# Optimization experiments

Measured on AMD Instinct MI355X. Metric: run time of the kernel, lower is better.

The kernel has to match this reference:

```python
import jax, jax.numpy as jnp
import numpy as np

SEQ = 4096
BLOCK = 64            # sparse_block_size
BLOCKS = SEQ // BLOCK # 64 block rows/cols
NUM_ORACLES = 32
ORACLE = SEQ // NUM_ORACLES      # 128
LOCAL_BLOCKS = ORACLE // BLOCK   # 2 (sliding-window width in blocks)
PATTERN_ID = 0


def _build_block_mask(pattern_id=PATTERN_ID):
    # Mirrors DKernelPredefinedSparseAttention.__init__ create_mask((i,))
    q_pos = np.arange(BLOCKS)[:, None]
    k_pos = np.arange(BLOCKS)[None, :]
    causal = q_pos >= k_pos
    sliding = (q_pos - k_pos) < LOCAL_BLOCKS
    vert = np.zeros(BLOCKS, dtype=bool)
    real_col = int(pattern_id * ORACLE + 0.5)
    cs = real_col // BLOCK
    ce = (real_col + ORACLE) // BLOCK
    vert[cs:ce] = True
    vert[0:1] = True  # global block 0 always visible
    return causal & (sliding | vert[None, :])


def setup_inputs() -> dict:
    key = jax.random.key(0)
    kq, kk, kv = jax.random.split(key, 3)
    shape = (1, SEQ, 8, 128)  # bshd, matches module's own smoke test layout
    q = jax.random.normal(kq, shape, dtype=jnp.float32)
    k = jax.random.normal(kk, shape, dtype=jnp.float32)
    v = jax.random.normal(kv, shape, dtype=jnp.float32)
    block_mask = jnp.asarray(_build_block_mask())  # [BLOCKS, BLOCKS] bool
    return {"q": q, "k": k, "v": v, "block_mask": block_mask}


def reference(q, k, v, block_mask):
    # Expand block-level mask to token level: [S, S]
    tok_mask = jnp.repeat(jnp.repeat(block_mask, BLOCK, axis=0), BLOCK, axis=1)
    scale = 1.0 / jnp.sqrt(jnp.asarray(q.shape[-1], q.dtype))
    # bshd x bshd -> bhqk scores
    scores = jnp.einsum("bqhd,bkhd->bhqk", q, k) * scale
    neg = jnp.asarray(-1e30, scores.dtype)
    scores = jnp.where(tok_mask[None, None, :, :], scores, neg)
    probs = jax.nn.softmax(scores, axis=-1)
    out = jnp.einsum("bhqk,bkhd->bqhd", probs, v)
    return out
```

## Files before the change

### kernel.cpp

```cpp
#include <hip/hip_runtime.h>
#include <hip/hip_bf16.h>

typedef __bf16 bf16x8 __attribute__((ext_vector_type(8)));
typedef float floatx4 __attribute__((ext_vector_type(4)));

constexpr int SEQ = 4096;
constexpr int NH  = 8;
constexpr int DH  = 128;
constexpr int BLK = 64;
constexpr int QBLOCKS = SEQ / BLK;
constexpr int RS = NH * DH;
constexpr float SCALE = 0.088388347648318447f;

__device__ __forceinline__ bf16x8 load8f(const float* p) {
    float4 a = *(const float4*)p;
    float4 b = *(const float4*)(p + 4);
    bf16x8 r = { (__bf16)a.x, (__bf16)a.y, (__bf16)a.z, (__bf16)a.w,
                 (__bf16)b.x, (__bf16)b.y, (__bf16)b.z, (__bf16)b.w };
    return r;
}

__device__ __forceinline__ void stage_v(const float* __restrict__ V,
                                        int kb, int h, int n_t, int kh,
                                        __bf16* __restrict__ dst) {
    const float* base = V + (size_t)(kb * BLK + kh * 32) * RS + h * DH + n_t;
    const int nt = n_t >> 4;
    const int lbase = n_t & 15;
#pragma unroll
    for (int g = 0; g < 4; ++g) {
        bf16x8 pk;
#pragma unroll
        for (int j = 0; j < 8; ++j)
            pk[j] = (__bf16)base[(size_t)(g * 8 + j) * RS];
        __bf16* d = dst + ((size_t)((kh * 8 + nt) * 64 + lbase + 16 * g)) * 8;
        *(bf16x8*)d = pk;
    }
}

__global__ __launch_bounds__(256) void sparse_attn_kernel(
    const float* __restrict__ Q,
    const float* __restrict__ K,
    const float* __restrict__ V,
    float* __restrict__ Out)
{
    const int qb   = blockIdx.x;
    const int h    = blockIdx.y;
    const int tid  = threadIdx.x;
    const int wave = tid >> 6;
    const int lane = tid & 63;
    const int quad = lane >> 4;
    const int l16  = lane & 15;

    __shared__ __align__(16) __bf16 v_lds[2][2][8][64][8];
    __shared__ __align__(16) __bf16 p_lds[4][16][BLK + 8];

    const int n_t = tid & 127;
    const int kh  = tid >> 7;

    const int qrow = qb * BLK + wave * 16 + l16;
    const float* qp = Q + (size_t)qrow * RS + h * DH;
    bf16x8 qfrag[4];
#pragma unroll
    for (int s = 0; s < 4; ++s)
        qfrag[s] = load8f(qp + s * 32 + quad * 8);

    floatx4 o_acc[8];
#pragma unroll
    for (int n = 0; n < 8; ++n) o_acc[n] = floatx4{0.f, 0.f, 0.f, 0.f};
    float m_run[4], l_run[4];
#pragma unroll
    for (int r = 0; r < 4; ++r) { m_run[r] = -1e30f; l_run[r] = 0.f; }

    int blist[4];
    int nb = 0;
    {
        int cand[4] = {0, 1, qb - 1, qb};
        for (int i = 0; i < 4; ++i) {
            int b = cand[i];
            if (b < 0 || b > qb) continue;
            bool dup = false;
            for (int j = 0; j < nb; ++j) dup = dup || (blist[j] == b);
            if (!dup) blist[nb++] = b;
        }
    }

    stage_v(V, blist[0], h, n_t, kh, &v_lds[0][0][0][0][0]);

    for (int bi = 0; bi < nb; ++bi) {
        __syncthreads();
        if (bi + 1 < nb)
            stage_v(V, blist[bi + 1], h, n_t, kh,
                    &v_lds[(bi + 1) & 1][0][0][0][0]);

        const int kb  = blist[bi];
        const int buf = bi & 1;

        floatx4 sfrag[4];
#pragma unroll
        for (int n = 0; n < 4; ++n) {
            floatx4 c = floatx4{0.f, 0.f, 0.f, 0.f};
            const float* kp =
                K + (size_t)(kb * BLK + n * 16 + l16) * RS + h * DH;
#pragma unroll
            for (int s = 0; s < 4; ++s) {
                bf16x8 kf = load8f(kp + s * 32 + quad * 8);
                c = __builtin_amdgcn_mfma_f32_16x16x32_bf16(qfrag[s], kf, c, 0, 0, 0);
            }
            sfrag[n] = c;
        }

        float mnew[4];
#pragma unroll
        for (int r = 0; r < 4; ++r) {
            float mx = m_run[r];
#pragma unroll
            for (int n = 0; n < 4; ++n) {
                sfrag[n][r] *= SCALE;
                mx = fmaxf(mx, sfrag[n][r]);
            }
#pragma unroll
            for (int off = 1; off < 16; off <<= 1)
                mx = fmaxf(mx, __shfl_xor(mx, off, 64));
            mnew[r] = mx;
        }
#pragma unroll
        for (int r = 0; r < 4; ++r) {
            float alpha = __expf(m_run[r] - mnew[r]);
            float rs = 0.f;
#pragma unroll
            for (int n = 0; n < 4; ++n) {
                float p = __expf(sfrag[n][r] - mnew[r]);
                sfrag[n][r] = p;
                rs += p;
            }
#pragma unroll
            for (int off = 1; off < 16; off <<= 1)
                rs += __shfl_xor(rs, off, 64);
            l_run[r] = l_run[r] * alpha + rs;
            m_run[r] = mnew[r];
#pragma unroll
            for (int n = 0; n < 8; ++n) o_acc[n][r] *= alpha;
        }

#pragma unroll
        for (int n = 0; n < 4; ++n)
#pragma unroll
            for (int r = 0; r < 4; ++r)
                p_lds[wave][quad * 4 + r][n * 16 + l16] = (__bf16)sfrag[n][r];

#pragma unroll
        for (int s2 = 0; s2 < 2; ++s2) {
            bf16x8 pa = *(const bf16x8*)&p_lds[wave][l16][s2 * 32 + quad * 8];
#pragma unroll
            for (int n = 0; n < 8; ++n) {
                bf16x8 vb = *(const bf16x8*)&v_lds[buf][s2][n][lane][0];
                o_acc[n] = __builtin_amdgcn_mfma_f32_16x16x32_bf16(pa, vb, o_acc[n], 0, 0, 0);
            }
        }
    }

    const int orow_base = qb * BLK + wave * 16 + quad * 4;
#pragma unroll
    for (int r = 0; r < 4; ++r) {
        float inv = 1.f / l_run[r];
        float* op = Out + (size_t)(orow_base + r) * RS + h * DH + l16;
#pragma unroll
        for (int n = 0; n < 8; ++n)
            op[n * 16] = o_acc[n][r] * inv;
    }
}

extern "C" void kernel_launch(void* const* d_in, const int* in_sizes, int n_in,
                              void* d_out, int out_size, void* d_ws, size_t ws_size,
                              hipStream_t stream) {
    const float* Q = (const float*)d_in[0];
    const float* K = (const float*)d_in[1];
    const float* V = (const float*)d_in[2];
    float* Out = (float*)d_out;

    dim3 grid(QBLOCKS, NH);
    dim3 block(256);
    sparse_attn_kernel<<<grid, block, 0, stream>>>(Q, K, V, Out);
}
```

Before: 125.9 us.

## Split KV blocks across two wave groups per workgroup and merge partial softmax

Doubles the workgroup to 512 threads and splits the up-to-four visible key blocks between two groups of four waves. Each group keeps its own online-softmax state, and the partial outputs are merged through LDS at the end. This shortens the serial per-workgroup loop over key blocks, which matters because the grid has only 512 workgroups. In exchange it drops the double-buffered V prefetch, adds a combine step with extra LDS traffic and barriers, and each Q row is loaded by both groups.

```diff
diff --git a/kernel.cpp b/kernel.cpp
--- a/kernel.cpp
+++ b/kernel.cpp
@@ -12,6 +12,8 @@
 constexpr int RS = NH * DH;
 constexpr float SCALE = 0.088388347648318447f;
 
+constexpr int SMEM_BYTES = 51200;
+
 __device__ __forceinline__ bf16x8 load8f(const float* p) {
     float4 a = *(const float4*)p;
     float4 b = *(const float4*)(p + 4);
@@ -37,7 +39,7 @@
     }
 }
 
-__global__ __launch_bounds__(256) void sparse_attn_kernel(
+__global__ __launch_bounds__(512, 4) void sparse_attn_kernel(
     const float* __restrict__ Q,
     const float* __restrict__ K,
     const float* __restrict__ V,
@@ -47,17 +49,24 @@
     const int h    = blockIdx.y;
     const int tid  = threadIdx.x;
     const int wave = tid >> 6;
+    const int g    = wave >> 2;
+    const int ws   = wave & 3;
     const int lane = tid & 63;
     const int quad = lane >> 4;
     const int l16  = lane & 15;
 
-    __shared__ __align__(16) __bf16 v_lds[2][2][8][64][8];
-    __shared__ __align__(16) __bf16 p_lds[4][16][BLK + 8];
-
-    const int n_t = tid & 127;
-    const int kh  = tid >> 7;
-
-    const int qrow = qb * BLK + wave * 16 + l16;
+    __shared__ __align__(16) char smem[SMEM_BYTES];
+    __bf16* v_g    = (__bf16*)(smem + g * 16384);
+    __bf16* p_w    = (__bf16*)(smem + 32768 + wave * 2304);
+    float*  comb_O = (float*)smem;
+    float*  comb_m = (float*)(smem + 33792);
+    float*  comb_l = (float*)(smem + 34048);
+
+    const int tg  = tid & 255;
+    const int n_t = tg & 127;
+    const int kh  = tg >> 7;
+
+    const int qrow = qb * BLK + ws * 16 + l16;
     const float* qp = Q + (size_t)qrow * RS + h * DH;
     bf16x8 qfrag[4];
 #pragma unroll
@@ -84,89 +93,110 @@
         }
     }
 
-    stage_v(V, blist[0], h, n_t, kh, &v_lds[0][0][0][0][0]);
-
-    for (int bi = 0; bi < nb; ++bi) {
+#pragma unroll 1
+    for (int t = 0; t < 2; ++t) {
+        const int s    = 2 * g + t;
+        const bool valid = (s < nb);
+        const int kb   = valid ? blist[s] : 0;
+
+        if (valid) stage_v(V, kb, h, n_t, kh, v_g);
         __syncthreads();
-        if (bi + 1 < nb)
-            stage_v(V, blist[bi + 1], h, n_t, kh,
-                    &v_lds[(bi + 1) & 1][0][0][0][0]);
-
-        const int kb  = blist[bi];
-        const int buf = bi & 1;
-
-        floatx4 sfrag[4];
-#pragma unroll
-        for (int n = 0; n < 4; ++n) {
-            floatx4 c = floatx4{0.f, 0.f, 0.f, 0.f};
-            const float* kp =
-                K + (size_t)(kb * BLK + n * 16 + l16) * RS + h * DH;
-#pragma unroll
-            for (int s = 0; s < 4; ++s) {
-                bf16x8 kf = load8f(kp + s * 32 + quad * 8);
-                c = __builtin_amdgcn_mfma_f32_16x16x32_bf16(qfrag[s], kf, c, 0, 0, 0);
-            }
-            sfrag[n] = c;
-        }
-
-        float mnew[4];
+
+        if (valid) {
+            floatx4 sfrag[4];
+#pragma unroll
+            for (int n = 0; n < 4; ++n) {
+                floatx4 c = floatx4{0.f, 0.f, 0.f, 0.f};
+                const float* kp =
+                    K + (size_t)(kb * BLK + n * 16 + l16) * RS + h * DH;
+#pragma unroll
+                for (int sx = 0; sx < 4; ++sx) {
+                    bf16x8 kf = load8f(kp + sx * 32 + quad * 8);
+                    c = __builtin_amdgcn_mfma_f32_16x16x32_bf16(qfrag[sx], kf, c, 0, 0, 0);
+                }
+                sfrag[n] = c;
+            }
+
+            float mnew[4];
+#pragma unroll
+            for (int r = 0; r < 4; ++r) {
+                float mx = m_run[r];
+#pragma unroll
+                for (int n = 0; n < 4; ++n) {
+                    sfrag[n][r] *= SCALE;
+                    mx = fmaxf(mx, sfrag[n][r]);
+                }
+#pragma unroll
+                for (int off = 1; off < 16; off <<= 1)
+                    mx = fmaxf(mx, __shfl_xor(mx, off, 64));
+                mnew[r] = mx;
+            }
+#pragma unroll
+            for (int r = 0; r < 4; ++r) {
+                float alpha = __expf(m_run[r] - mnew[r]);
+                float rs = 0.f;
+#pragma unroll
+                for (int n = 0; n < 4; ++n) {
+                    float p = __expf(sfrag[n][r] - mnew[r]);
+                    sfrag[n][r] = p;
+                    rs += p;
+                }
+#pragma unroll
+                for (int off = 1; off < 16; off <<= 1)
+                    rs += __shfl_xor(rs, off, 64);
+                l_run[r] = l_run[r] * alpha + rs;
+                m_run[r] = mnew[r];
+#pragma unroll
+                for (int n = 0; n < 8; ++n) o_acc[n][r] *= alpha;
+            }
+
+#pragma unroll
+            for (int n = 0; n < 4; ++n)
+#pragma unroll
+                for (int r = 0; r < 4; ++r)
+                    p_w[(quad * 4 + r) * 72 + n * 16 + l16] = (__bf16)sfrag[n][r];
+
+#pragma unroll
+            for (int s2 = 0; s2 < 2; ++s2) {
+                bf16x8 pa = *(const bf16x8*)&p_w[l16 * 72 + s2 * 32 + quad * 8];
+#pragma unroll
+                for (int n = 0; n < 8; ++n) {
+                    bf16x8 vb = *(const bf16x8*)&v_g[((s2 * 8 + n) * 64 + lane) * 8];
+                    o_acc[n] = __builtin_amdgcn_mfma_f32_16x16x32_bf16(pa, vb, o_acc[n], 0, 0, 0);
+                }
+            }
+        }
+        __syncthreads();
+    }
+
+    if (g == 1) {
 #pragma unroll
         for (int r = 0; r < 4; ++r) {
-            float mx = m_run[r];
-#pragma unroll
-            for (int n = 0; n < 4; ++n) {
-                sfrag[n][r] *= SCALE;
-                mx = fmaxf(mx, sfrag[n][r]);
-            }
-#pragma unroll
-            for (int off = 1; off < 16; off <<= 1)
-                mx = fmaxf(mx, __shfl_xor(mx, off, 64));
-            mnew[r] = mx;
-        }
+            const int row = ws * 16 + quad * 4 + r;
+#pragma unroll
+            for (int n = 0; n < 8; ++n)
+                comb_O[row * 132 + n * 16 + l16] = o_acc[n][r];
+            comb_m[row] = m_run[r];
+            comb_l[row] = l_run[r];
+        }
+    }
+    __syncthreads();
+    if (g == 0) {
 #pragma unroll
         for (int r = 0; r < 4; ++r) {
-            float alpha = __expf(m_run[r] - mnew[r]);
-            float rs = 0.f;
-#pragma unroll
-            for (int n = 0; n < 4; ++n) {
-                float p = __expf(sfrag[n][r] - mnew[r]);
-                sfrag[n][r] = p;
-                rs += p;
-            }
-#pragma unroll
-            for (int off = 1; off < 16; off <<= 1)
-                rs += __shfl_xor(rs, off, 64);
-            l_run[r] = l_run[r] * alpha + rs;
-            m_run[r] = mnew[r];
-#pragma unroll
-            for (int n = 0; n < 8; ++n) o_acc[n][r] *= alpha;
-        }
-
-#pragma unroll
-        for (int n = 0; n < 4; ++n)
-#pragma unroll
-            for (int r = 0; r < 4; ++r)
-                p_lds[wave][quad * 4 + r][n * 16 + l16] = (__bf16)sfrag[n][r];
-
-#pragma unroll
-        for (int s2 = 0; s2 < 2; ++s2) {
-            bf16x8 pa = *(const bf16x8*)&p_lds[wave][l16][s2 * 32 + quad * 8];
-#pragma unroll
-            for (int n = 0; n < 8; ++n) {
-                bf16x8 vb = *(const bf16x8*)&v_lds[buf][s2][n][lane][0];
-                o_acc[n] = __builtin_amdgcn_mfma_f32_16x16x32_bf16(pa, vb, o_acc[n], 0, 0, 0);
-            }
-        }
-    }
-
-    const int orow_base = qb * BLK + wave * 16 + quad * 4;
-#pragma unroll
-    for (int r = 0; r < 4; ++r) {
-        float inv = 1.f / l_run[r];
-        float* op = Out + (size_t)(orow_base + r) * RS + h * DH + l16;
-#pragma unroll
-        for (int n = 0; n < 8; ++n)
-            op[n * 16] = o_acc[n][r] * inv;
+            const int row = ws * 16 + quad * 4 + r;
+            const float m1 = comb_m[row];
+            const float l1 = comb_l[row];
+            const float ms = fmaxf(m_run[r], m1);
+            const float f0 = __expf(m_run[r] - ms);
+            const float f1 = __expf(m1 - ms);
+            const float linv = 1.f / (f0 * l_run[r] + f1 * l1);
+            float* op = Out + (size_t)(qb * BLK + row) * RS + h * DH + l16;
+#pragma unroll
+            for (int n = 0; n < 8; ++n)
+                op[n * 16] = (f0 * o_acc[n][r] +
+                              f1 * comb_O[row * 132 + n * 16 + l16]) * linv;
+        }
     }
 }
 
@@ -179,6 +209,6 @@
     float* Out = (float*)d_out;
 
     dim3 grid(QBLOCKS, NH);
-    dim3 block(256);
+    dim3 block(512);
     sparse_attn_kernel<<<grid, block, 0, stream>>>(Q, K, V, Out);
 }
```

Result: slower. 128.8 us (+2.3%).
